# Performance work log

Hardware: AMD Instinct MI355X
Metric: run time of the kernel (lower is better)

Reference implementation:

```python
import jax, jax.numpy as jnp
import numpy as np
from jax import lax

KS = 3
N = KS ** 3  # 27 kernel taps


def setup_inputs() -> dict:
    key = jax.random.key(0)
    k1, k2, k3 = jax.random.split(key, 3)
    B, Cin, Cout, D, H, W = 1, 32, 32, 32, 48, 48
    x = jax.random.normal(k1, (B, Cin, D, H, W), jnp.float32)
    # offset conv: 81 = 3*27 output channels, no bias (nn.Conv3d(..., bias=False))
    w_off = jax.random.normal(k2, (3 * N, Cin, KS, KS, KS), jnp.float32) * 0.01
    # deform conv kernel (bias defaults to None -> no bias)
    w_def = jax.random.normal(k3, (Cout, Cin, KS, KS, KS), jnp.float32) / np.sqrt(Cin * N)
    return {"x": x, "w_off": w_off, "w_def": w_def}


def _deform_block(x, w_off, w_def):
    B, C, D, H, W = x.shape
    dt = x.dtype

    # standard dense offset conv, padding=1
    offsets = lax.conv_general_dilated(
        x, w_off, (1, 1, 1), [(1, 1), (1, 1), (1, 1)],
        dimension_numbers=("NCDHW", "OIDHW", "NCDHW"))
    off = jnp.transpose(offsets, (0, 2, 3, 4, 1))  # (B,D,H,W,3N)
    od, oh, ow = off[..., :N], off[..., N:2 * N], off[..., 2 * N:]

    # zero-pad input (ConstantPad3d(1))
    xp = jnp.pad(x, ((0, 0), (0, 0), (1, 1), (1, 1), (1, 1)))
    Dp, Hp, Wp = D + 2, H + 2, W + 2

    # p_n: kernel grid offsets in (kd,kh,kw) row-major order, matching conv-weight layout
    r = jnp.arange(-(KS // 2), KS // 2 + 1, dtype=dt)
    pn = jnp.stack(jnp.meshgrid(r, r, r, indexing="ij"), 0).reshape(3, N)
    # p_0: centers in padded coordinates (1..D etc.)
    p0d = jnp.arange(1, D + 1, dtype=dt)[:, None, None, None]
    p0h = jnp.arange(1, H + 1, dtype=dt)[None, :, None, None]
    p0w = jnp.arange(1, W + 1, dtype=dt)[None, None, :, None]

    pd = p0d + pn[0] + od  # (B,D,H,W,N) sampling coords
    ph = p0h + pn[1] + oh
    pw = p0w + pn[2] + ow

    # integer corners (detached in original)
    fd = lax.stop_gradient(jnp.floor(pd))
    fh = lax.stop_gradient(jnp.floor(ph))
    fw = lax.stop_gradient(jnp.floor(pw))
    qd0 = jnp.clip(fd, 0, Dp - 1); qd1 = jnp.clip(fd + 1, 0, Dp - 1)
    qh0 = jnp.clip(fh, 0, Hp - 1); qh1 = jnp.clip(fh + 1, 0, Hp - 1)
    qw0 = jnp.clip(fw, 0, Wp - 1); qw1 = jnp.clip(fw + 1, 0, Wp - 1)

    # clip p to valid range (as in reference impl)
    pd = jnp.clip(pd, 0, Dp - 1)
    ph = jnp.clip(ph, 0, Hp - 1)
    pw = jnp.clip(pw, 0, Wp - 1)

    # trilinear weights per axis: g = 1 - |q - p|
    gd0 = 1 + (qd0 - pd); gd1 = 1 - (qd1 - pd)
    gh0 = 1 + (qh0 - ph); gh1 = 1 - (qh1 - ph)
    gw0 = 1 + (qw0 - pw); gw1 = 1 - (qw1 - pw)

    xf = xp.reshape(B, C, Dp * Hp * Wp)

    def gather(idd, ihh, iww):
        lin = ((idd.astype(jnp.int32) * Hp + ihh.astype(jnp.int32)) * Wp
               + iww.astype(jnp.int32)).reshape(B, 1, -1)
        v = jnp.take_along_axis(xf, jnp.broadcast_to(lin, (B, C, lin.shape[-1])), axis=2)
        return v.reshape(B, C, D, H, W, N)

    x_off = jnp.zeros((B, C, D, H, W, N), dt)
    for gd, idd in ((gd0, qd0), (gd1, qd1)):
        for gh, ihh in ((gh0, qh0), (gh1, qh1)):
            for gw, iww in ((gw0, qw0), (gw1, qw1)):
                x_off = x_off + (gd * gh * gw)[:, None] * gather(idd, ihh, iww)

    # stride-ks conv over reshaped x_offset == weighted sum over the N taps
    Cout = w_def.shape[0]
    out = jnp.einsum("bcdhwn,ocn->bodhw", x_off, w_def.reshape(Cout, C, N))
    return out


def reference(x, w_off, w_def):
    return _deform_block(x, w_off, w_def)
```

## Files before the change

kernel.cpp:

```cpp
#include <hip/hip_runtime.h>

typedef __attribute__((ext_vector_type(8))) short  short8;
typedef __attribute__((ext_vector_type(4))) float  f32x4;
typedef __attribute__((ext_vector_type(2))) float  f32x2;

#define CIN 32
#define COUT 32
#define DD 32
#define HH 48
#define WW 48
#define NTAP 27
#define SPATIAL (DD*HH*WW)

#define BP2_ELEMS (27*6*64*8)
#define OFF_WPK   ((size_t)BP2_ELEMS*2)
#define WPK_ELEMS (27*2*64*8)
#define OFF_XT    (OFF_WPK + (size_t)WPK_ELEMS*2)

#define SB0() __builtin_amdgcn_sched_barrier(0)

__device__ __forceinline__ unsigned short f2bf(float f) {
    union { float f; unsigned u; } v; v.f = f;
    unsigned r = v.u + 0x7FFFu + ((v.u >> 16) & 1u);
    return (unsigned short)(r >> 16);
}
__device__ __forceinline__ float bitsf(unsigned u) {
    union { unsigned u; float f; } v; v.u = u; return v.f;
}

__global__ __launch_bounds__(256) void wprep2_kernel(
        const float* __restrict__ w_off, unsigned short* __restrict__ Bp2)
{
    int i = blockIdx.x * 256 + threadIdx.x;
    if (i >= BP2_ELEMS) return;
    int e    = i & 7;
    int lane = (i >> 3) & 63;
    int j    = (i >> 9) % 6;
    int n    = i / (512 * 6);
    int col = lane & 15, kg = lane >> 4;
    int oc = j * 16 + col, c = kg * 8 + e;
    float v = (oc < 81) ? w_off[((size_t)oc * CIN + c) * NTAP + n] : 0.f;
    Bp2[i] = f2bf(v);
}

__global__ __launch_bounds__(256) void wdefprep_kernel(
        const float* __restrict__ w_def, unsigned short* __restrict__ wpk)
{
    int i = blockIdx.x * 256 + threadIdx.x;
    if (i >= WPK_ELEMS) return;
    int e    = i & 7;
    int lane = (i >> 3) & 63;
    int half = (i >> 9) & 1;
    int n    = i >> 10;
    int kg = lane >> 4, col = lane & 15;
    int c  = kg * 8 + e, oc = half * 16 + col;
    wpk[i] = f2bf(w_def[((size_t)oc * CIN + c) * NTAP + n]);
}

__global__ __launch_bounds__(256) void xtrans_kernel(
        const float* __restrict__ x, unsigned short* __restrict__ xT)
{
    __shared__ float t[CIN][65];
    const int p0 = blockIdx.x * 64;
    const int tid = threadIdx.x;
    const int tx = tid & 63, ty = tid >> 6;
    #pragma unroll
    for (int k = 0; k < 8; ++k) {
        int c = ty + k * 4;
        t[c][tx] = x[(size_t)c * SPATIAL + p0 + tx];
    }
    __syncthreads();
    const int pl = tid >> 2, cg = (tid & 3) * 8;
    short8 v;
    #pragma unroll
    for (int i = 0; i < 8; ++i) v[i] = (short)f2bf(t[cg + i][pl]);
    *(short8*)&xT[((size_t)(p0 + pl)) * 32 + cg] = v;
}

struct ConvT {
    uint4 a;
    uint4 wt[6];
    int   valid;
};

struct Gath {
    uint4 cw[8];
    uint4 wb0, wb1;
    float gg[8];
};

__device__ __forceinline__ void conv_issue(
        ConvT& ct, const uint4* __restrict__ Xu, const uint4* __restrict__ Bu,
        int n, int pos, int d, int h, int w, int kg, int lane)
{
    int td = n / 9, th = (n / 3) % 3, tw = n % 3;
    int valid = ((unsigned)(d + td - 1) < DD)
              & ((unsigned)(h + th - 1) < HH)
              & ((unsigned)(w + tw - 1) < WW);
    int dpos = pos + (td - 1) * 2304 + (th - 1) * 48 + (tw - 1);
    int safe = valid ? dpos : pos;
    ct.a = Xu[(size_t)safe * 4 + kg];
    #pragma unroll
    for (int j = 0; j < 6; ++j)
        ct.wt[j] = Bu[(size_t)(n * 6 + j) * 64 + lane];
    ct.valid = valid;
}

__device__ __forceinline__ void conv_consume(const ConvT& ct, f32x4* cacc)
{
    uint4 a = ct.a;
    if (!ct.valid) { a.x = 0; a.y = 0; a.z = 0; a.w = 0; }
    union { uint4 u; short8 s; } av; av.u = a;
    #pragma unroll
    for (int j = 0; j < 6; ++j) {
        union { uint4 u; short8 s; } b; b.u = ct.wt[j];
        cacc[j] = __builtin_amdgcn_mfma_f32_16x16x32_bf16(av.s, b.s, cacc[j], 0, 0, 0);
    }
}

__device__ __forceinline__ void tap_issue(
        Gath& tb, const uint4* __restrict__ Xu, const uint4* __restrict__ Wu,
        float od, float oh, float ow,
        int n, int d, int h, int w, int kg, int lane)
{
    float rd = (float)(n / 9) - 1.f;
    float rh = (float)((n / 3) % 3) - 1.f;
    float rw = (float)(n % 3) - 1.f;

    float pdp = (float)(d + 1) + rd + od;
    float php = (float)(h + 1) + rh + oh;
    float pwp = (float)(w + 1) + rw + ow;

    float fd = floorf(pdp), fh = floorf(php), fw = floorf(pwp);
    float qd0 = fminf(fmaxf(fd,       0.f), 33.f);
    float qd1 = fminf(fmaxf(fd + 1.f, 0.f), 33.f);
    float qh0 = fminf(fmaxf(fh,       0.f), 49.f);
    float qh1 = fminf(fmaxf(fh + 1.f, 0.f), 49.f);
    float qw0 = fminf(fmaxf(fw,       0.f), 49.f);
    float qw1 = fminf(fmaxf(fw + 1.f, 0.f), 49.f);
    float pcd = fminf(fmaxf(pdp, 0.f), 33.f);
    float pch = fminf(fmaxf(php, 0.f), 49.f);
    float pcw = fminf(fmaxf(pwp, 0.f), 49.f);

    float gd0 = 1.f + (qd0 - pcd), gd1 = 1.f - (qd1 - pcd);
    float gh0 = 1.f + (qh0 - pch), gh1 = 1.f - (qh1 - pch);
    float gw0 = 1.f + (qw0 - pcw), gw1 = 1.f - (qw1 - pcw);
    gd0 = (qd0 >= 1.f && qd0 <= 32.f) ? gd0 : 0.f;
    gd1 = (qd1 >= 1.f && qd1 <= 32.f) ? gd1 : 0.f;
    gh0 = (qh0 >= 1.f && qh0 <= 48.f) ? gh0 : 0.f;
    gh1 = (qh1 >= 1.f && qh1 <= 48.f) ? gh1 : 0.f;
    gw0 = (qw0 >= 1.f && qw0 <= 48.f) ? gw0 : 0.f;
    gw1 = (qw1 >= 1.f && qw1 <= 48.f) ? gw1 : 0.f;
    int zd0 = (int)fminf(fmaxf(qd0, 1.f), 32.f) - 1;
    int zd1 = (int)fminf(fmaxf(qd1, 1.f), 32.f) - 1;
    int zh0 = (int)fminf(fmaxf(qh0, 1.f), 48.f) - 1;
    int zh1 = (int)fminf(fmaxf(qh1, 1.f), 48.f) - 1;
    int zw0 = (int)fminf(fmaxf(qw0, 1.f), 48.f) - 1;
    int zw1 = (int)fminf(fmaxf(qw1, 1.f), 48.f) - 1;

    int bd0 = zd0 * 2304, bd1 = zd1 * 2304;
    int bh0 = zh0 * 48,   bh1 = zh1 * 48;
    float gdh00 = gd0 * gh0, gdh01 = gd0 * gh1;
    float gdh10 = gd1 * gh0, gdh11 = gd1 * gh1;

    tb.cw[0] = Xu[(size_t)(bd0 + bh0 + zw0) * 4 + kg];
    tb.cw[1] = Xu[(size_t)(bd0 + bh0 + zw1) * 4 + kg];
    tb.cw[2] = Xu[(size_t)(bd0 + bh1 + zw0) * 4 + kg];
    tb.cw[3] = Xu[(size_t)(bd0 + bh1 + zw1) * 4 + kg];
    tb.cw[4] = Xu[(size_t)(bd1 + bh0 + zw0) * 4 + kg];
    tb.cw[5] = Xu[(size_t)(bd1 + bh0 + zw1) * 4 + kg];
    tb.cw[6] = Xu[(size_t)(bd1 + bh1 + zw0) * 4 + kg];
    tb.cw[7] = Xu[(size_t)(bd1 + bh1 + zw1) * 4 + kg];
    tb.wb0   = Wu[(size_t)(n * 2 + 0) * 64 + lane];
    tb.wb1   = Wu[(size_t)(n * 2 + 1) * 64 + lane];

    tb.gg[0] = gdh00 * gw0;  tb.gg[1] = gdh00 * gw1;
    tb.gg[2] = gdh01 * gw0;  tb.gg[3] = gdh01 * gw1;
    tb.gg[4] = gdh10 * gw0;  tb.gg[5] = gdh10 * gw1;
    tb.gg[6] = gdh11 * gw0;  tb.gg[7] = gdh11 * gw1;
}

__device__ __forceinline__ void tap_consume(
        const Gath& tb, f32x4& acc0, f32x4& acc1)
{
    f32x2 xa0 = {0.f, 0.f}, xa1 = {0.f, 0.f};
    f32x2 xa2 = {0.f, 0.f}, xa3 = {0.f, 0.f};

    #pragma unroll
    for (int e = 0; e < 8; ++e) {
        uint4 cw = tb.cw[e];
        f32x2 g2 = {tb.gg[e], tb.gg[e]};
        f32x2 v0 = {bitsf(cw.x << 16), bitsf(cw.x & 0xFFFF0000u)};
        f32x2 v1 = {bitsf(cw.y << 16), bitsf(cw.y & 0xFFFF0000u)};
        f32x2 v2 = {bitsf(cw.z << 16), bitsf(cw.z & 0xFFFF0000u)};
        f32x2 v3 = {bitsf(cw.w << 16), bitsf(cw.w & 0xFFFF0000u)};
        asm("v_pk_fma_f32 %0, %1, %2, %0" : "+v"(xa0) : "v"(v0), "v"(g2));
        asm("v_pk_fma_f32 %0, %1, %2, %0" : "+v"(xa1) : "v"(v1), "v"(g2));
        asm("v_pk_fma_f32 %0, %1, %2, %0" : "+v"(xa2) : "v"(v2), "v"(g2));
        asm("v_pk_fma_f32 %0, %1, %2, %0" : "+v"(xa3) : "v"(v3), "v"(g2));
    }

    union { unsigned u[4]; short8 s; } av;
    asm("v_cvt_pk_bf16_f32 %0, %1, %2" : "=v"(av.u[0]) : "v"(xa0.x), "v"(xa0.y));
    asm("v_cvt_pk_bf16_f32 %0, %1, %2" : "=v"(av.u[1]) : "v"(xa1.x), "v"(xa1.y));
    asm("v_cvt_pk_bf16_f32 %0, %1, %2" : "=v"(av.u[2]) : "v"(xa2.x), "v"(xa2.y));
    asm("v_cvt_pk_bf16_f32 %0, %1, %2" : "=v"(av.u[3]) : "v"(xa3.x), "v"(xa3.y));

    union { uint4 u; short8 s; } b0, b1;
    b0.u = tb.wb0; b1.u = tb.wb1;
    acc0 = __builtin_amdgcn_mfma_f32_16x16x32_bf16(av.s, b0.s, acc0, 0, 0, 0);
    acc1 = __builtin_amdgcn_mfma_f32_16x16x32_bf16(av.s, b1.s, acc1, 0, 0, 0);
}

__global__ __launch_bounds__(128, 3) void fused_deform6(
        const unsigned short* __restrict__ xT,
        const unsigned short* __restrict__ Bp2,
        const unsigned short* __restrict__ wpk,
        float* __restrict__ out)
{
    __shared__ float offl[2][16][97];

    const int tid  = threadIdx.x;
    const int lane = tid & 63, wv = tid >> 6;
    const int p0   = blockIdx.x * 32 + wv * 16;
    const int kg   = lane >> 4;
    const int row  = lane & 15;
    const int pos  = p0 + row;
    const int w = pos % WW, h = (pos / WW) % HH, d = pos / (WW * HH);

    const uint4* Xu = (const uint4*)xT;
    const uint4* Bu = (const uint4*)Bp2;
    const uint4* Wu = (const uint4*)wpk;

    f32x4 cacc[6];
    #pragma unroll
    for (int j = 0; j < 6; ++j) cacc[j] = (f32x4){0.f, 0.f, 0.f, 0.f};

    {
        ConvT cA, cB;
        conv_issue(cA, Xu, Bu, 0, pos, d, h, w, kg, lane);
        SB0();
        #pragma unroll 1
        for (int n = 0; n < 26; n += 2) {
            conv_issue(cB, Xu, Bu, n + 1, pos, d, h, w, kg, lane);
            SB0();
            conv_consume(cA, cacc);
            conv_issue(cA, Xu, Bu, n + 2, pos, d, h, w, kg, lane);
            SB0();
            conv_consume(cB, cacc);
        }
        conv_consume(cA, cacc);
    }

    #pragma unroll
    for (int j = 0; j < 6; ++j) {
        #pragma unroll
        for (int r = 0; r < 4; ++r)
            offl[wv][kg * 4 + r][j * 16 + row] = cacc[j][r];
    }
    __syncthreads();

    const float* ol = &offl[wv][row][0];

    f32x4 acc0 = {0.f, 0.f, 0.f, 0.f};
    f32x4 acc1 = {0.f, 0.f, 0.f, 0.f};

    {
        Gath gA, gB;
        float odA = ol[0], ohA = ol[27], owA = ol[54];
        tap_issue(gA, Xu, Wu, odA, ohA, owA, 0, d, h, w, kg, lane);
        SB0();
        float odB = ol[1], ohB = ol[28], owB = ol[55];

        #pragma unroll 1
        for (int n = 0; n < 26; n += 2) {
            tap_issue(gB, Xu, Wu, odB, ohB, owB, n + 1, d, h, w, kg, lane);
            SB0();
            odA = ol[n + 2]; ohA = ol[27 + n + 2]; owA = ol[54 + n + 2];
            tap_consume(gA, acc0, acc1);
            tap_issue(gA, Xu, Wu, odA, ohA, owA, n + 2, d, h, w, kg, lane);
            SB0();
            int nb = (n + 3 < 27) ? n + 3 : 26;
            odB = ol[nb]; ohB = ol[27 + nb]; owB = ol[54 + nb];
            tap_consume(gB, acc0, acc1);
        }
        tap_consume(gA, acc0, acc1);
    }

    const int pb = p0 + kg * 4;
    *(f32x4*)&out[(size_t)row        * SPATIAL + pb] = acc0;
    *(f32x4*)&out[(size_t)(16 + row) * SPATIAL + pb] = acc1;
}

extern "C" void kernel_launch(void* const* d_in, const int* in_sizes, int n_in,
                              void* d_out, int out_size, void* d_ws, size_t ws_size,
                              hipStream_t stream)
{
    const float* x     = (const float*)d_in[0];
    const float* w_off = (const float*)d_in[1];
    const float* w_def = (const float*)d_in[2];
    float* out = (float*)d_out;

    unsigned short* Bp2 = (unsigned short*)((char*)d_ws);
    unsigned short* wpk = (unsigned short*)((char*)d_ws + OFF_WPK);
    unsigned short* xT  = (unsigned short*)((char*)d_ws + OFF_XT);

    wprep2_kernel<<<(BP2_ELEMS + 255) / 256, 256, 0, stream>>>(w_off, Bp2);
    wdefprep_kernel<<<(WPK_ELEMS + 255) / 256, 256, 0, stream>>>(w_def, wpk);
    xtrans_kernel<<<SPATIAL / 64, 256, 0, stream>>>(x, xT);
    fused_deform6<<<SPATIAL / 32, 128, 0, stream>>>(xT, Bp2, wpk, out);
}
```

Before: 135.0 us.

## Stage per-tap weights in shared memory cooperatively across four waves

Blocks grow from two to four waves (64 positions). Per-tap B fragments for the offset conv and the deform MFMA are no longer loaded by every wave from global memory. Each wave now loads a slice, writes it into double-buffered LDS, and all waves read the full tile after a barrier, so global/L2 weight traffic per position drops. The cost is an extra LDS round trip plus a block-wide barrier per tap, which couples the waves and may stall the gather pipelining. The weight workspaces are padded to power-of-two strides per tap.

```diff
diff --git a/kernel.cpp b/kernel.cpp
--- a/kernel.cpp
+++ b/kernel.cpp
@@ -12,12 +12,16 @@
 #define NTAP 27
 #define SPATIAL (DD*HH*WW)
 
-#define BP2_ELEMS (27*6*64*8)
-#define OFF_WPK   ((size_t)BP2_ELEMS*2)
-#define WPK_ELEMS (27*2*64*8)
-#define OFF_XT    (OFF_WPK + (size_t)WPK_ELEMS*2)
+#define BP2_BYTES (27*8192)
+#define OFF_WPK   ((size_t)BP2_BYTES)
+#define WPK_BYTES (27*4096)
+#define OFF_XT    (OFF_WPK + WPK_BYTES)
 
 #define SB0() __builtin_amdgcn_sched_barrier(0)
+#define LGKM0_BAR() do { \
+    asm volatile("s_waitcnt lgkmcnt(0)" ::: "memory"); \
+    __builtin_amdgcn_s_barrier(); \
+    SB0(); } while (0)
 
 __device__ __forceinline__ unsigned short f2bf(float f) {
     union { float f; unsigned u; } v; v.f = f;
@@ -32,7 +36,7 @@
         const float* __restrict__ w_off, unsigned short* __restrict__ Bp2)
 {
     int i = blockIdx.x * 256 + threadIdx.x;
-    if (i >= BP2_ELEMS) return;
+    if (i >= 27 * 6 * 64 * 8) return;
     int e    = i & 7;
     int lane = (i >> 3) & 63;
     int j    = (i >> 9) % 6;
@@ -40,21 +44,22 @@
     int col = lane & 15, kg = lane >> 4;
     int oc = j * 16 + col, c = kg * 8 + e;
     float v = (oc < 81) ? w_off[((size_t)oc * CIN + c) * NTAP + n] : 0.f;
-    Bp2[i] = f2bf(v);
+    Bp2[(size_t)n * 4096 + (j * 64 + lane) * 8 + e] = f2bf(v);
 }
 
 __global__ __launch_bounds__(256) void wdefprep_kernel(
         const float* __restrict__ w_def, unsigned short* __restrict__ wpk)
 {
     int i = blockIdx.x * 256 + threadIdx.x;
-    if (i >= WPK_ELEMS) return;
+    if (i >= 27 * 2 * 64 * 8) return;
     int e    = i & 7;
     int lane = (i >> 3) & 63;
     int half = (i >> 9) & 1;
     int n    = i >> 10;
     int kg = lane >> 4, col = lane & 15;
     int c  = kg * 8 + e, oc = half * 16 + col;
-    wpk[i] = f2bf(w_def[((size_t)oc * CIN + c) * NTAP + n]);
+    wpk[(size_t)n * 2048 + (half * 64 + lane) * 8 + e] =
+        f2bf(w_def[((size_t)oc * CIN + c) * NTAP + n]);
 }
 
 __global__ __launch_bounds__(256) void xtrans_kernel(
@@ -77,51 +82,15 @@
     *(short8*)&xT[((size_t)(p0 + pl)) * 32 + cg] = v;
 }
 
-struct ConvT {
-    uint4 a;
-    uint4 wt[6];
-    int   valid;
-};
-
 struct Gath {
     uint4 cw[8];
-    uint4 wb0, wb1;
     float gg[8];
 };
 
-__device__ __forceinline__ void conv_issue(
-        ConvT& ct, const uint4* __restrict__ Xu, const uint4* __restrict__ Bu,
-        int n, int pos, int d, int h, int w, int kg, int lane)
-{
-    int td = n / 9, th = (n / 3) % 3, tw = n % 3;
-    int valid = ((unsigned)(d + td - 1) < DD)
-              & ((unsigned)(h + th - 1) < HH)
-              & ((unsigned)(w + tw - 1) < WW);
-    int dpos = pos + (td - 1) * 2304 + (th - 1) * 48 + (tw - 1);
-    int safe = valid ? dpos : pos;
-    ct.a = Xu[(size_t)safe * 4 + kg];
-    #pragma unroll
-    for (int j = 0; j < 6; ++j)
-        ct.wt[j] = Bu[(size_t)(n * 6 + j) * 64 + lane];
-    ct.valid = valid;
-}
-
-__device__ __forceinline__ void conv_consume(const ConvT& ct, f32x4* cacc)
-{
-    uint4 a = ct.a;
-    if (!ct.valid) { a.x = 0; a.y = 0; a.z = 0; a.w = 0; }
-    union { uint4 u; short8 s; } av; av.u = a;
-    #pragma unroll
-    for (int j = 0; j < 6; ++j) {
-        union { uint4 u; short8 s; } b; b.u = ct.wt[j];
-        cacc[j] = __builtin_amdgcn_mfma_f32_16x16x32_bf16(av.s, b.s, cacc[j], 0, 0, 0);
-    }
-}
-
 __device__ __forceinline__ void tap_issue(
-        Gath& tb, const uint4* __restrict__ Xu, const uint4* __restrict__ Wu,
+        Gath& tb, const uint4* __restrict__ Xu,
         float od, float oh, float ow,
-        int n, int d, int h, int w, int kg, int lane)
+        int n, int d, int h, int w, int kg)
 {
     float rd = (float)(n / 9) - 1.f;
     float rh = (float)((n / 3) % 3) - 1.f;
@@ -171,8 +140,6 @@
     tb.cw[5] = Xu[(size_t)(bd1 + bh0 + zw1) * 4 + kg];
     tb.cw[6] = Xu[(size_t)(bd1 + bh1 + zw0) * 4 + kg];
     tb.cw[7] = Xu[(size_t)(bd1 + bh1 + zw1) * 4 + kg];
-    tb.wb0   = Wu[(size_t)(n * 2 + 0) * 64 + lane];
-    tb.wb1   = Wu[(size_t)(n * 2 + 1) * 64 + lane];
 
     tb.gg[0] = gdh00 * gw0;  tb.gg[1] = gdh00 * gw1;
     tb.gg[2] = gdh01 * gw0;  tb.gg[3] = gdh01 * gw1;
@@ -181,7 +148,7 @@
 }
 
 __device__ __forceinline__ void tap_consume(
-        const Gath& tb, f32x4& acc0, f32x4& acc1)
+        const Gath& tb, short8 b0, short8 b1, f32x4& acc0, f32x4& acc1)
 {
     f32x2 xa0 = {0.f, 0.f}, xa1 = {0.f, 0.f};
     f32x2 xa2 = {0.f, 0.f}, xa3 = {0.f, 0.f};
@@ -206,50 +173,86 @@
     asm("v_cvt_pk_bf16_f32 %0, %1, %2" : "=v"(av.u[2]) : "v"(xa2.x), "v"(xa2.y));
     asm("v_cvt_pk_bf16_f32 %0, %1, %2" : "=v"(av.u[3]) : "v"(xa3.x), "v"(xa3.y));
 
-    union { uint4 u; short8 s; } b0, b1;
-    b0.u = tb.wb0; b1.u = tb.wb1;
-    acc0 = __builtin_amdgcn_mfma_f32_16x16x32_bf16(av.s, b0.s, acc0, 0, 0, 0);
-    acc1 = __builtin_amdgcn_mfma_f32_16x16x32_bf16(av.s, b1.s, acc1, 0, 0, 0);
-}
-
-__global__ __launch_bounds__(128, 3) void fused_deform6(
+    acc0 = __builtin_amdgcn_mfma_f32_16x16x32_bf16(av.s, b0, acc0, 0, 0, 0);
+    acc1 = __builtin_amdgcn_mfma_f32_16x16x32_bf16(av.s, b1, acc1, 0, 0, 0);
+}
+
+__global__ __launch_bounds__(256, 3) void fused_deform7(
         const unsigned short* __restrict__ xT,
         const unsigned short* __restrict__ Bp2,
         const unsigned short* __restrict__ wpk,
         float* __restrict__ out)
 {
-    __shared__ float offl[2][16][97];
+    __shared__ float offl[4][16][97];
+    __shared__ __align__(16) char convB[2][8192];
+    __shared__ __align__(16) char ebuf[2][4096];
 
     const int tid  = threadIdx.x;
     const int lane = tid & 63, wv = tid >> 6;
-    const int p0   = blockIdx.x * 32 + wv * 16;
+    const int p0   = blockIdx.x * 64 + wv * 16;
     const int kg   = lane >> 4;
     const int row  = lane & 15;
     const int pos  = p0 + row;
     const int w = pos % WW, h = (pos / WW) % HH, d = pos / (WW * HH);
 
     const uint4* Xu = (const uint4*)xT;
-    const uint4* Bu = (const uint4*)Bp2;
-    const uint4* Wu = (const uint4*)wpk;
+    const char*  Bb = (const char*)Bp2;
+    const char*  Wb = (const char*)wpk;
 
     f32x4 cacc[6];
     #pragma unroll
     for (int j = 0; j < 6; ++j) cacc[j] = (f32x4){0.f, 0.f, 0.f, 0.f};
 
+    auto loadA = [&](int n, int& valid) -> uint4 {
+        int td = n / 9, th = (n / 3) % 3, tw = n % 3;
+        valid = ((unsigned)(d + td - 1) < DD)
+              & ((unsigned)(h + th - 1) < HH)
+              & ((unsigned)(w + tw - 1) < WW);
+        int dpos = pos + (td - 1) * 2304 + (th - 1) * 48 + (tw - 1);
+        int safe = valid ? dpos : pos;
+        return Xu[(size_t)safe * 4 + kg];
+    };
+    auto loadBc = [&](int n, uint4* br) {
+        const char* src = Bb + (size_t)n * 8192 + (wv * 2) * 1024 + lane * 16;
+        br[0] = *(const uint4*)(src);
+        br[1] = *(const uint4*)(src + 1024);
+    };
+    auto writeBc = [&](int buf, const uint4* br) {
+        char* dst = &convB[buf][(wv * 2) * 1024 + lane * 16];
+        *(uint4*)(dst)        = br[0];
+        *(uint4*)(dst + 1024) = br[1];
+    };
+    auto consumeConv = [&](int buf, uint4 a, int valid) {
+        if (!valid) { a.x = 0; a.y = 0; a.z = 0; a.w = 0; }
+        union { uint4 u; short8 s; } av; av.u = a;
+        #pragma unroll
+        for (int j = 0; j < 6; ++j) {
+            short8 b = *(const short8*)&convB[buf][(j * 64 + lane) * 16];
+            cacc[j] = __builtin_amdgcn_mfma_f32_16x16x32_bf16(av.s, b, cacc[j], 0, 0, 0);
+        }
+    };
+
     {
-        ConvT cA, cB;
-        conv_issue(cA, Xu, Bu, 0, pos, d, h, w, kg, lane);
-        SB0();
+        uint4 brA[2], brB[2], aA, aB;
+        int vA, vB;
+        loadBc(0, brA);  aA = loadA(0, vA);
         #pragma unroll 1
         for (int n = 0; n < 26; n += 2) {
-            conv_issue(cB, Xu, Bu, n + 1, pos, d, h, w, kg, lane);
+            loadBc(n + 1, brB);  aB = loadA(n + 1, vB);
             SB0();
-            conv_consume(cA, cacc);
-            conv_issue(cA, Xu, Bu, n + 2, pos, d, h, w, kg, lane);
+            writeBc(n & 1, brA);
+            LGKM0_BAR();
+            consumeConv(n & 1, aA, vA);
+            loadBc(n + 2, brA);  aA = loadA(n + 2, vA);
             SB0();
-            conv_consume(cB, cacc);
+            writeBc((n + 1) & 1, brB);
+            LGKM0_BAR();
+            consumeConv((n + 1) & 1, aB, vB);
         }
-        conv_consume(cA, cacc);
+        SB0();
+        writeBc(0, brA);
+        LGKM0_BAR();
+        consumeConv(0, aA, vA);
     }
 
     #pragma unroll
@@ -265,26 +268,48 @@
     f32x4 acc0 = {0.f, 0.f, 0.f, 0.f};
     f32x4 acc1 = {0.f, 0.f, 0.f, 0.f};
 
+    auto loadEB = [&](int n) -> uint4 {
+        return *(const uint4*)(Wb + (size_t)n * 4096 + wv * 1024 + lane * 16);
+    };
+    auto writeEB = [&](int buf, uint4 v) {
+        *(uint4*)&ebuf[buf][wv * 1024 + lane * 16] = v;
+    };
+    auto consumeTap = [&](int buf, const Gath& g) {
+        short8 b0 = *(const short8*)&ebuf[buf][lane * 16];
+        short8 b1 = *(const short8*)&ebuf[buf][1024 + lane * 16];
+        tap_consume(g, b0, b1, acc0, acc1);
+    };
+
     {
         Gath gA, gB;
+        uint4 ebA, ebB;
         float odA = ol[0], ohA = ol[27], owA = ol[54];
-        tap_issue(gA, Xu, Wu, odA, ohA, owA, 0, d, h, w, kg, lane);
-        SB0();
+        ebA = loadEB(0);
+        tap_issue(gA, Xu, odA, ohA, owA, 0, d, h, w, kg);
         float odB = ol[1], ohB = ol[28], owB = ol[55];
 
         #pragma unroll 1
         for (int n = 0; n < 26; n += 2) {
-            tap_issue(gB, Xu, Wu, odB, ohB, owB, n + 1, d, h, w, kg, lane);
+            ebB = loadEB(n + 1);
+            tap_issue(gB, Xu, odB, ohB, owB, n + 1, d, h, w, kg);
+            odA = ol[n + 2]; ohA = ol[27 + n + 2]; owA = ol[54 + n + 2];
             SB0();
-            odA = ol[n + 2]; ohA = ol[27 + n + 2]; owA = ol[54 + n + 2];
-            tap_consume(gA, acc0, acc1);
-            tap_issue(gA, Xu, Wu, odA, ohA, owA, n + 2, d, h, w, kg, lane);
-            SB0();
+            writeEB(n & 1, ebA);
+            LGKM0_BAR();
+            consumeTap(n & 1, gA);
+            ebA = loadEB(n + 2);
+            tap_issue(gA, Xu, odA, ohA, owA, n + 2, d, h, w, kg);
             int nb = (n + 3 < 27) ? n + 3 : 26;
             odB = ol[nb]; ohB = ol[27 + nb]; owB = ol[54 + nb];
-            tap_consume(gB, acc0, acc1);
+            SB0();
+            writeEB((n + 1) & 1, ebB);
+            LGKM0_BAR();
+            consumeTap((n + 1) & 1, gB);
         }
-        tap_consume(gA, acc0, acc1);
+        SB0();
+        writeEB(0, ebA);
+        LGKM0_BAR();
+        consumeTap(0, gA);
     }
 
     const int pb = p0 + kg * 4;
@@ -305,8 +330,8 @@
     unsigned short* wpk = (unsigned short*)((char*)d_ws + OFF_WPK);
     unsigned short* xT  = (unsigned short*)((char*)d_ws + OFF_XT);
 
-    wprep2_kernel<<<(BP2_ELEMS + 255) / 256, 256, 0, stream>>>(w_off, Bp2);
-    wdefprep_kernel<<<(WPK_ELEMS + 255) / 256, 256, 0, stream>>>(w_def, wpk);
+    wprep2_kernel<<<(27 * 6 * 64 * 8 + 255) / 256, 256, 0, stream>>>(w_off, Bp2);
+    wdefprep_kernel<<<(27 * 2 * 64 * 8 + 255) / 256, 256, 0, stream>>>(w_def, wpk);
     xtrans_kernel<<<SPATIAL / 64, 256, 0, stream>>>(x, xT);
-    fused_deform6<<<SPATIAL / 32, 128, 0, stream>>>(xT, Bp2, wpk, out);
-}
+    fused_deform7<<<SPATIAL / 64, 256, 0, stream>>>(xT, Bp2, wpk, out);
+}
```

Result: slower. 187.2 us (+38.7%).

## Process two 16-position tiles per wave to reuse weight loads, swizzle blocks

Applied to the files above, without the earlier changes.

Each wave now handles 32 spatial positions as two 16-row MFMA tiles, so every weight fragment loaded for the offset conv and the deform conv is shared across two tiles. The explicit A/B double-buffered software pipeline is replaced by a simple per-tap loop that relies on the doubled independent work for latency hiding. Block IDs are remapped across 8 groups, presumably to spread neighbouring positions across XCDs or caches. Register pressure rises, so the occupancy hint drops from 3 to 2 blocks per SIMD, and the grid is halved, which risks less latency hiding.

```diff
diff --git a/kernel.cpp b/kernel.cpp
--- a/kernel.cpp
+++ b/kernel.cpp
@@ -77,51 +77,15 @@
     *(short8*)&xT[((size_t)(p0 + pl)) * 32 + cg] = v;
 }
 
-struct ConvT {
-    uint4 a;
-    uint4 wt[6];
-    int   valid;
-};
-
 struct Gath {
     uint4 cw[8];
-    uint4 wb0, wb1;
     float gg[8];
 };
 
-__device__ __forceinline__ void conv_issue(
-        ConvT& ct, const uint4* __restrict__ Xu, const uint4* __restrict__ Bu,
-        int n, int pos, int d, int h, int w, int kg, int lane)
-{
-    int td = n / 9, th = (n / 3) % 3, tw = n % 3;
-    int valid = ((unsigned)(d + td - 1) < DD)
-              & ((unsigned)(h + th - 1) < HH)
-              & ((unsigned)(w + tw - 1) < WW);
-    int dpos = pos + (td - 1) * 2304 + (th - 1) * 48 + (tw - 1);
-    int safe = valid ? dpos : pos;
-    ct.a = Xu[(size_t)safe * 4 + kg];
-    #pragma unroll
-    for (int j = 0; j < 6; ++j)
-        ct.wt[j] = Bu[(size_t)(n * 6 + j) * 64 + lane];
-    ct.valid = valid;
-}
-
-__device__ __forceinline__ void conv_consume(const ConvT& ct, f32x4* cacc)
-{
-    uint4 a = ct.a;
-    if (!ct.valid) { a.x = 0; a.y = 0; a.z = 0; a.w = 0; }
-    union { uint4 u; short8 s; } av; av.u = a;
-    #pragma unroll
-    for (int j = 0; j < 6; ++j) {
-        union { uint4 u; short8 s; } b; b.u = ct.wt[j];
-        cacc[j] = __builtin_amdgcn_mfma_f32_16x16x32_bf16(av.s, b.s, cacc[j], 0, 0, 0);
-    }
-}
-
 __device__ __forceinline__ void tap_issue(
-        Gath& tb, const uint4* __restrict__ Xu, const uint4* __restrict__ Wu,
+        Gath& tb, const uint4* __restrict__ Xu,
         float od, float oh, float ow,
-        int n, int d, int h, int w, int kg, int lane)
+        int n, int d, int h, int w, int kg)
 {
     float rd = (float)(n / 9) - 1.f;
     float rh = (float)((n / 3) % 3) - 1.f;
@@ -171,8 +135,6 @@
     tb.cw[5] = Xu[(size_t)(bd1 + bh0 + zw1) * 4 + kg];
     tb.cw[6] = Xu[(size_t)(bd1 + bh1 + zw0) * 4 + kg];
     tb.cw[7] = Xu[(size_t)(bd1 + bh1 + zw1) * 4 + kg];
-    tb.wb0   = Wu[(size_t)(n * 2 + 0) * 64 + lane];
-    tb.wb1   = Wu[(size_t)(n * 2 + 1) * 64 + lane];
 
     tb.gg[0] = gdh00 * gw0;  tb.gg[1] = gdh00 * gw1;
     tb.gg[2] = gdh01 * gw0;  tb.gg[3] = gdh01 * gw1;
@@ -181,7 +143,7 @@
 }
 
 __device__ __forceinline__ void tap_consume(
-        const Gath& tb, f32x4& acc0, f32x4& acc1)
+        const Gath& tb, short8 b0, short8 b1, f32x4& acc0, f32x4& acc1)
 {
     f32x2 xa0 = {0.f, 0.f}, xa1 = {0.f, 0.f};
     f32x2 xa2 = {0.f, 0.f}, xa3 = {0.f, 0.f};
@@ -206,90 +168,113 @@
     asm("v_cvt_pk_bf16_f32 %0, %1, %2" : "=v"(av.u[2]) : "v"(xa2.x), "v"(xa2.y));
     asm("v_cvt_pk_bf16_f32 %0, %1, %2" : "=v"(av.u[3]) : "v"(xa3.x), "v"(xa3.y));
 
-    union { uint4 u; short8 s; } b0, b1;
-    b0.u = tb.wb0; b1.u = tb.wb1;
-    acc0 = __builtin_amdgcn_mfma_f32_16x16x32_bf16(av.s, b0.s, acc0, 0, 0, 0);
-    acc1 = __builtin_amdgcn_mfma_f32_16x16x32_bf16(av.s, b1.s, acc1, 0, 0, 0);
-}
-
-__global__ __launch_bounds__(128, 3) void fused_deform6(
+    acc0 = __builtin_amdgcn_mfma_f32_16x16x32_bf16(av.s, b0, acc0, 0, 0, 0);
+    acc1 = __builtin_amdgcn_mfma_f32_16x16x32_bf16(av.s, b1, acc1, 0, 0, 0);
+}
+
+__global__ __launch_bounds__(128, 2) void fused_deform9(
         const unsigned short* __restrict__ xT,
         const unsigned short* __restrict__ Bp2,
         const unsigned short* __restrict__ wpk,
         float* __restrict__ out)
 {
-    __shared__ float offl[2][16][97];
+    __shared__ float offl[2][2][16][82];
+
+    const int bid  = (int)blockIdx.x;
+    const int sbid = (bid & 7) * 144 + (bid >> 3);
 
     const int tid  = threadIdx.x;
     const int lane = tid & 63, wv = tid >> 6;
-    const int p0   = blockIdx.x * 32 + wv * 16;
+    const int p0   = sbid * 64 + wv * 32;
     const int kg   = lane >> 4;
     const int row  = lane & 15;
-    const int pos  = p0 + row;
-    const int w = pos % WW, h = (pos / WW) % HH, d = pos / (WW * HH);
+    const int pos0 = p0 + row;
+    const int pos1 = p0 + 16 + row;
+    const int w0c = pos0 % WW, h0c = (pos0 / WW) % HH, d0c = pos0 / (WW * HH);
+    const int w1c = pos1 % WW, h1c = (pos1 / WW) % HH, d1c = pos1 / (WW * HH);
 
     const uint4* Xu = (const uint4*)xT;
     const uint4* Bu = (const uint4*)Bp2;
     const uint4* Wu = (const uint4*)wpk;
 
-    f32x4 cacc[6];
-    #pragma unroll
-    for (int j = 0; j < 6; ++j) cacc[j] = (f32x4){0.f, 0.f, 0.f, 0.f};
+    f32x4 cacc0[6], cacc1[6];
+    #pragma unroll
+    for (int j = 0; j < 6; ++j) {
+        cacc0[j] = (f32x4){0.f, 0.f, 0.f, 0.f};
+        cacc1[j] = (f32x4){0.f, 0.f, 0.f, 0.f};
+    }
 
     {
-        ConvT cA, cB;
-        conv_issue(cA, Xu, Bu, 0, pos, d, h, w, kg, lane);
-        SB0();
         #pragma unroll 1
-        for (int n = 0; n < 26; n += 2) {
-            conv_issue(cB, Xu, Bu, n + 1, pos, d, h, w, kg, lane);
+        for (int n = 0; n < NTAP; ++n) {
+            int td = n / 9, th = (n / 3) % 3, tw = n % 3;
+            int dis = (td - 1) * 2304 + (th - 1) * 48 + (tw - 1);
+            int v0 = ((unsigned)(d0c + td - 1) < DD) & ((unsigned)(h0c + th - 1) < HH)
+                   & ((unsigned)(w0c + tw - 1) < WW);
+            int v1 = ((unsigned)(d1c + td - 1) < DD) & ((unsigned)(h1c + th - 1) < HH)
+                   & ((unsigned)(w1c + tw - 1) < WW);
+            uint4 a0 = Xu[(size_t)(v0 ? pos0 + dis : pos0) * 4 + kg];
+            uint4 a1 = Xu[(size_t)(v1 ? pos1 + dis : pos1) * 4 + kg];
+            uint4 wt[6];
+            #pragma unroll
+            for (int j = 0; j < 6; ++j)
+                wt[j] = Bu[(size_t)(n * 6 + j) * 64 + lane];
             SB0();
-            conv_consume(cA, cacc);
-            conv_issue(cA, Xu, Bu, n + 2, pos, d, h, w, kg, lane);
-            SB0();
-            conv_consume(cB, cacc);
+            if (!v0) { a0.x = 0; a0.y = 0; a0.z = 0; a0.w = 0; }
+            if (!v1) { a1.x = 0; a1.y = 0; a1.z = 0; a1.w = 0; }
+            union { uint4 u; short8 s; } av0, av1, b;
+            av0.u = a0; av1.u = a1;
+            #pragma unroll
+            for (int j = 0; j < 6; ++j) {
+                b.u = wt[j];
+                cacc0[j] = __builtin_amdgcn_mfma_f32_16x16x32_bf16(av0.s, b.s, cacc0[j], 0, 0, 0);
+                cacc1[j] = __builtin_amdgcn_mfma_f32_16x16x32_bf16(av1.s, b.s, cacc1[j], 0, 0, 0);
+            }
         }
-        conv_consume(cA, cacc);
     }
 
     #pragma unroll
     for (int j = 0; j < 6; ++j) {
         #pragma unroll
-        for (int r = 0; r < 4; ++r)
-            offl[wv][kg * 4 + r][j * 16 + row] = cacc[j][r];
+        for (int r = 0; r < 4; ++r) {
+            int col = j * 16 + row;
+            if (col < 81) {
+                offl[wv][0][kg * 4 + r][col] = cacc0[j][r];
+                offl[wv][1][kg * 4 + r][col] = cacc1[j][r];
+            }
+        }
     }
     __syncthreads();
 
-    const float* ol = &offl[wv][row][0];
-
-    f32x4 acc0 = {0.f, 0.f, 0.f, 0.f};
-    f32x4 acc1 = {0.f, 0.f, 0.f, 0.f};
+    const float* ol0 = &offl[wv][0][row][0];
+    const float* ol1 = &offl[wv][1][row][0];
+
+    f32x4 acc00 = {0.f, 0.f, 0.f, 0.f}, acc01 = {0.f, 0.f, 0.f, 0.f};
+    f32x4 acc10 = {0.f, 0.f, 0.f, 0.f}, acc11 = {0.f, 0.f, 0.f, 0.f};
 
     {
-        Gath gA, gB;
-        float odA = ol[0], ohA = ol[27], owA = ol[54];
-        tap_issue(gA, Xu, Wu, odA, ohA, owA, 0, d, h, w, kg, lane);
-        SB0();
-        float odB = ol[1], ohB = ol[28], owB = ol[55];
-
+        Gath g0, g1;
         #pragma unroll 1
-        for (int n = 0; n < 26; n += 2) {
-            tap_issue(gB, Xu, Wu, odB, ohB, owB, n + 1, d, h, w, kg, lane);
+        for (int n = 0; n < NTAP; ++n) {
+            uint4 wbu0 = Wu[(size_t)(n * 2 + 0) * 64 + lane];
+            uint4 wbu1 = Wu[(size_t)(n * 2 + 1) * 64 + lane];
+            tap_issue(g0, Xu, ol0[n], ol0[27 + n], ol0[54 + n], n, d0c, h0c, w0c, kg);
             SB0();
-            odA = ol[n + 2]; ohA = ol[27 + n + 2]; owA = ol[54 + n + 2];
-            tap_consume(gA, acc0, acc1);
-            tap_issue(gA, Xu, Wu, odA, ohA, owA, n + 2, d, h, w, kg, lane);
+            tap_issue(g1, Xu, ol1[n], ol1[27 + n], ol1[54 + n], n, d1c, h1c, w1c, kg);
             SB0();
-            int nb = (n + 3 < 27) ? n + 3 : 26;
-            odB = ol[nb]; ohB = ol[27 + nb]; owB = ol[54 + nb];
-            tap_consume(gB, acc0, acc1);
+            union { uint4 u; short8 s; } b0, b1;
+            b0.u = wbu0; b1.u = wbu1;
+            tap_consume(g0, b0.s, b1.s, acc00, acc01);
+            tap_consume(g1, b0.s, b1.s, acc10, acc11);
         }
-        tap_consume(gA, acc0, acc1);
-    }
-
-    const int pb = p0 + kg * 4;
-    *(f32x4*)&out[(size_t)row        * SPATIAL + pb] = acc0;
-    *(f32x4*)&out[(size_t)(16 + row) * SPATIAL + pb] = acc1;
+    }
+
+    const int pb0 = p0 + kg * 4;
+    const int pb1 = p0 + 16 + kg * 4;
+    *(f32x4*)&out[(size_t)row        * SPATIAL + pb0] = acc00;
+    *(f32x4*)&out[(size_t)(16 + row) * SPATIAL + pb0] = acc01;
+    *(f32x4*)&out[(size_t)row        * SPATIAL + pb1] = acc10;
+    *(f32x4*)&out[(size_t)(16 + row) * SPATIAL + pb1] = acc11;
 }
 
 extern "C" void kernel_launch(void* const* d_in, const int* in_sizes, int n_in,
@@ -308,5 +293,5 @@
     wprep2_kernel<<<(BP2_ELEMS + 255) / 256, 256, 0, stream>>>(w_off, Bp2);
     wdefprep_kernel<<<(WPK_ELEMS + 255) / 256, 256, 0, stream>>>(w_def, wpk);
     xtrans_kernel<<<SPATIAL / 64, 256, 0, stream>>>(x, xT);
-    fused_deform6<<<SPATIAL / 32, 128, 0, stream>>>(xT, Bp2, wpk, out);
-}
+    fused_deform9<<<SPATIAL / 64, 128, 0, stream>>>(xT, Bp2, wpk, out);
+}
```

Result: faster. 123.9 us (-8.2%).
